# Kernel tuning notes

Measured on AMD Instinct MI355X. Metric: run time of the kernel, lower is better.

Reference implementation:

```python
import jax, jax.numpy as jnp
import numpy as np

LMAX = 4
S2_DIM = (LMAX + 1) ** 2                                  # 25: s2 irreps, mul 1 per l
SO3_DIM = sum((2 * l + 1) ** 2 for l in range(LMAX + 1))  # 165: so3 irreps, mul 2l+1 per l
B = 2048
F_S2, F_SO3 = 1, 16
N_S2_KERNEL = 48      # s2_healpix_grid(rec_level=1)
N_SO3_KERNEL = 192    # so3_near_identity_grid()
N_ACT_GRID = 4000     # SO3Activation resolution=10, aspect_ratio=2 -> 20x10x20, flattened
N_EVAL = 4608         # so3_healpix_grid(rec_level=2): 192 pixels x 24 gamma


def setup_inputs() -> dict:
    ks = jax.random.split(jax.random.key(0), 7)
    return {
        "x": jax.random.normal(ks[0], (B, F_S2, S2_DIM), jnp.float32),
        "w_s2": jax.random.normal(ks[1], (F_S2, F_SO3, N_S2_KERNEL), jnp.float32),
        "Y": jax.random.normal(ks[2], (N_S2_KERNEL, S2_DIM), jnp.float32),
        "w_so3": jax.random.normal(ks[3], (F_SO3, 1, N_SO3_KERNEL), jnp.float32),
        "D_kernel": jax.random.normal(ks[4], (N_SO3_KERNEL, SO3_DIM), jnp.float32),
        "D_act": jax.random.normal(ks[5], (N_ACT_GRID, SO3_DIM), jnp.float32),
        "eval_wigners": jax.random.normal(ks[6], (SO3_DIM, N_EVAL), jnp.float32) / np.sqrt(SO3_DIM),
    }


def _s2_to_so3_linear(x, psi):
    # e3nn o3.Linear(s2_irreps -> so3_irreps, f_in, f_out, external weights)
    # x:   [B, f_in, 25]  (mul 1 per degree l)
    # psi: [f_in, f_out, 25] ; column l^2+j is the weight to output-multiplicity j of degree l
    f_in, f_out = psi.shape[0], psi.shape[1]
    out, s = [], 0
    for l in range(LMAX + 1):
        d = 2 * l + 1
        x_l = x[..., s:s + d]                       # [B, f_in, d]
        p_l = psi[..., s:s + d]                     # [f_in, f_out, d] (j = out-mul idx)
        o = jnp.einsum('bxm,xyj->byjm', x_l, p_l) / np.sqrt(f_in)
        out.append(o.reshape(x.shape[0], f_out, d * d))
        s += d
    return jnp.concatenate(out, axis=-1)            # [B, f_out, 165]


def _so3_to_so3_linear(x, psi):
    # e3nn o3.Linear(so3_irreps -> so3_irreps, f_in, f_out, external weights)
    # x:   [B, f_in, 165] ; psi: [f_in, f_out, 165]
    f_in, f_out = psi.shape[0], psi.shape[1]
    out, s = [], 0
    for l in range(LMAX + 1):
        d = 2 * l + 1
        x_l = x[..., s:s + d * d].reshape(x.shape[0], f_in, d, d)   # [B,f_in,u,m]
        p_l = psi[..., s:s + d * d].reshape(f_in, f_out, d, d)      # [f_in,f_out,u,v]
        o = jnp.einsum('bxum,xyuv->byvm', x_l, p_l) / np.sqrt(f_in * d)
        out.append(o.reshape(x.shape[0], f_out, d * d))
        s += d * d
    return jnp.concatenate(out, axis=-1)            # [B, f_out, 165]


def _forward(x, w_s2, Y, w_so3, D_kernel, D_act, eval_wigners):
    # --- S2Convolution: kernel = SH-transform of grid weights, then irrep-wise linear
    psi1 = jnp.einsum('ni,xyn->xyi', Y, w_s2) / np.sqrt(N_S2_KERNEL)     # [1,16,25]
    h = _s2_to_so3_linear(x, psi1)                                        # [B,16,165]
    # --- SO3Activation: Fourier -> SO(3) grid -> relu -> Fourier
    g = jnp.einsum('bfi,gi->bfg', h, D_act) / np.sqrt(SO3_DIM)            # [B,16,4000]
    g = jax.nn.relu(g)
    h = jnp.einsum('bfg,gi->bfi', g, D_act) * (np.sqrt(SO3_DIM) / N_ACT_GRID)
    # --- SO3Convolution
    psi2 = jnp.einsum('ni,xyn->xyi', D_kernel, w_so3) / np.sqrt(N_SO3_KERNEL)  # [16,1,165]
    harmonics = _so3_to_so3_linear(h, psi2)                               # [B,1,165]
    # --- compute_probabilities: matmul with eval Wigner-D basis + softmax over grid
    probs = jax.nn.softmax(jnp.einsum('bfi,ie->be', harmonics, eval_wigners), axis=1)  # [B,4608]
    # --- top-k masking: zero out everything below the 5th-highest prob of sample 0
    fifth = jax.lax.top_k(probs, 5)[0][0, 4]
    probs = jnp.where(probs < fifth, 0.0, probs)
    return harmonics, probs


def reference(x, w_s2, Y, w_so3, D_kernel, D_act, eval_wigners):
    return _forward(x, w_s2, Y, w_so3, D_kernel, D_act, eval_wigners)
```

## Files before the change

### kernel.cpp

```cpp
#include <hip/hip_runtime.h>

typedef short bf16x8 __attribute__((ext_vector_type(8)));
typedef float f32x16 __attribute__((ext_vector_type(16)));
typedef int   i32x4  __attribute__((ext_vector_type(4)));

#define INV_SQRT165 0.07784989441615349f
#define FINAL_SCALE 0.0032113081446662823f
#define ZERO16 ((f32x16){0.f,0.f,0.f,0.f,0.f,0.f,0.f,0.f,0.f,0.f,0.f,0.f,0.f,0.f,0.f,0.f})

__device__ __forceinline__ unsigned short f2bf(float f) {
  unsigned int u = __builtin_bit_cast(unsigned int, f);
  unsigned int r = (u + 0x7FFFu + ((u >> 16) & 1u)) >> 16;
  return (unsigned short)r;
}
__device__ __forceinline__ float bf2f(unsigned short h) {
  unsigned int u = ((unsigned int)h) << 16;
  return __builtin_bit_cast(float, u);
}

__device__ __forceinline__ void gl_lds16(const void* g, void* l) {
  __builtin_amdgcn_global_load_lds(
      (const __attribute__((address_space(1))) unsigned int*)(unsigned long long)g,
      (__attribute__((address_space(3))) unsigned int*)(unsigned int)(unsigned long long)l,
      16, 0, 0);
}

__device__ __forceinline__ void decode_i(int i, int& lv, int& rel) {
  if (i < 1)       { lv = 0; rel = i; }
  else if (i < 10) { lv = 1; rel = i - 1; }
  else if (i < 35) { lv = 2; rel = i - 10; }
  else if (i < 84) { lv = 3; rel = i - 35; }
  else             { lv = 4; rel = i - 84; }
}
__device__ __forceinline__ int divq(int rel, int lv) {
  const int mag[5] = {32768, 10923, 6554, 4682, 3641};
  return (rel * mag[lv]) >> 15;
}

__device__ __forceinline__ int gperm(int p) {
  int a = p & 3, hlp = (p >> 2) & 1, c = p >> 3;
  return ((c >> 1) << 4) + hlp * 8 + ((c & 1) << 2) + a;
}

__global__ __launch_bounds__(256) void prep_k(const float* __restrict__ Da,
                                              const float* __restrict__ ew,
                                              const float* __restrict__ Y,
                                              const float* __restrict__ w_s2,
                                              const float* __restrict__ Dk,
                                              const float* __restrict__ w_so3,
                                              unsigned short* __restrict__ e1pre,
                                              unsigned short* __restrict__ d2pre,
                                              unsigned short* __restrict__ ewpre,
                                              float* __restrict__ psi2) {
  __shared__ __align__(16) unsigned short lds[13824];
  const int tid = threadIdx.x;
  const int l = tid & 63, hl = l >> 5, ln = l & 31;
  if (blockIdx.x < 512) {
    const int ci = blockIdx.x >> 2, yg = blockIdx.x & 3;
    const int g0 = ci * 32;
    float* psi1L = (float*)(lds + 6464);
    for (int e = tid; e < 6400; e += 256) lds[e] = 0;
    for (int e = tid; e < 400; e += 256) {
      int yv = e / 25, iv = e % 25;
      float s = 0.f;
      for (int n = 0; n < 48; n++) s += Y[n * 25 + iv] * w_s2[yv * 48 + n];
      psi1L[e] = s * 0.14433756729740643f;
    }
    __syncthreads();
    int rows = 4000 - g0; if (rows > 32) rows = 32; if (rows < 0) rows = 0;
    int ne = rows * 165;
    for (int e = tid; e < ne; e += 256) {
      int gl_ = e / 165, k = e - gl_ * 165;
      lds[gl_ * 200 + k] = f2bf(Da[g0 * 165 + e]);
    }
    __syncthreads();
    if (yg == 0) {
#pragma unroll
      for (int it = 0; it < 3; it++) {
        int tt = it * 4 + (tid >> 6);
        int nf = tt >> 1, gk = tt & 1;
        unsigned short v[8];
#pragma unroll
        for (int j = 0; j < 8; j++)
          v[j] = lds[(gk * 16 + hl * 8 + j) * 200 + nf * 32 + ln];
        *(i32x4*)(d2pre + ci * 6144 + tt * 512 + l * 8) = *(i32x4*)v;
      }
    }
    for (int yi = 0; yi < 4; yi++) {
      int yy = yg * 4 + yi;
#pragma unroll
      for (int it = 0; it < 4; it++) {
        int idx = it * 256 + tid;
        int kf = idx >> 9, r2 = idx & 511;
        int ll = r2 >> 3, j = r2 & 7;
        int lnn = ll & 31, hll = ll >> 5;
        int k = kf * 16 + hll * 8 + j;
        unsigned short ov = 0;
        if (k < 25) {
          int lv = (k < 1) ? 0 : (k < 4) ? 1 : (k < 9) ? 2 : (k < 16) ? 3 : 4;
          int d = 2 * lv + 1;
          int m = k - lv * lv;
          int off165 = lv * (4 * lv * lv - 1) / 3;
          int gp = gperm(lnn);
          float s = 0.f;
          const float* pr = psi1L + yy * 25 + lv * lv;
          const unsigned short* dr = lds + gp * 200 + off165 + m;
          for (int j2 = 0; j2 < d; j2++) s += pr[j2] * bf2f(dr[j2 * d]);
          ov = f2bf(s * INV_SQRT165);
        }
        e1pre[((yy * 128 + ci) * 2 + kf) * 512 + ll * 8 + j] = ov;
      }
    }
  } else if (blockIdx.x < 584) {
    const int bx2 = blockIdx.x - 512;
    const int n0 = bx2 * 64;
    for (int e = tid; e < 13824; e += 256) lds[e] = 0;
    __syncthreads();
    for (int e = tid; e < 10560; e += 256) {
      int k = e >> 6, n = e & 63;
      lds[k * 72 + n] = f2bf(ew[k * 4608 + n0 + n]);
    }
    __syncthreads();
#pragma unroll
    for (int it = 0; it < 6; it++) {
      int tb = it * 4 + (tid >> 6);
      int nt2 = tb / 12, kf = tb - nt2 * 12;
      unsigned short v[8];
#pragma unroll
      for (int j = 0; j < 8; j++)
        v[j] = lds[(kf * 16 + hl * 8 + j) * 72 + nt2 * 32 + ln];
      *(i32x4*)(ewpre + (bx2 * 2 + nt2) * 6144 + kf * 512 + l * 8) = *(i32x4*)v;
    }
  } else {
    int t = (blockIdx.x - 584) * 256 + tid;
    if (t < 2640) {
      int ch = t / 165, i = t % 165;
      float s = 0.f;
      for (int n = 0; n < 192; n++) s += Dk[n * 165 + i] * w_so3[ch * 192 + n];
      psi2[t] = s * (0.07216878364870323f * FINAL_SCALE);
    }
  }
}

__global__ __launch_bounds__(256, 2) void fused_mlp_k(
    const float* __restrict__ x,
    const unsigned short* __restrict__ e1pre,
    const unsigned short* __restrict__ d2pre,
    unsigned short* __restrict__ part)
{
  __shared__ __align__(16) unsigned char smem[24576];
  const int tid = threadIdx.x;
  const int w = tid >> 6, l = tid & 63;
  const int hl = l >> 5, ln = l & 31;
  const int h = blockIdx.x >> 8;
  const int y = (blockIdx.x >> 4) & 15;
  const int btq = blockIdx.x & 15;
  const int btp = w & 1, nh = w >> 1;
  const int bt0 = btq * 4 + btp * 2;
  const int c0 = h * 63;
  const int cnt = h ? 62 : 63;

  bf16x8 xf0[2], xf1[2];
#pragma unroll
  for (int t = 0; t < 2; t++) {
    const float* xr = x + ((bt0 + t) * 32 + ln) * 25;
#pragma unroll
    for (int kf = 0; kf < 2; kf++) {
      unsigned short v[8];
#pragma unroll
      for (int j = 0; j < 8; j++) {
        int k = kf * 16 + hl * 8 + j;
        v[j] = (k < 25) ? f2bf(xr[k]) : (unsigned short)0;
      }
      if (t == 0) xf0[kf] = *(bf16x8*)v; else xf1[kf] = *(bf16x8*)v;
    }
  }

  f32x16 o0[3], o1[3];
#pragma unroll
  for (int i = 0; i < 3; i++) { o0[i] = ZERO16; o1[i] = ZERO16; }

  const unsigned short* ebase = e1pre + (y * 128) * 1024;

  bf16x8 eC0 = *(const bf16x8*)(ebase + (c0 * 2 + 0) * 512 + l * 8);
  bf16x8 eC1 = *(const bf16x8*)(ebase + (c0 * 2 + 1) * 512 + l * 8);
#pragma unroll
  for (int i = 0; i < 3; i++) {
    int tb = w + i * 4;
    gl_lds16(d2pre + c0 * 6144 + tb * 512 + l * 8, smem + tb * 1024);
  }

  for (int ci = 0; ci < cnt; ci++) {
    __syncthreads();
    const unsigned char* cb = smem + (ci & 1) * 12288;
    bf16x8 eN0 = eC0, eN1 = eC1;
    if (ci + 1 < cnt) {
      unsigned char* nb = smem + ((ci + 1) & 1) * 12288;
      const int c = c0 + ci + 1;
#pragma unroll
      for (int i = 0; i < 3; i++) {
        int tb = w + i * 4;
        gl_lds16(d2pre + c * 6144 + tb * 512 + l * 8, nb + tb * 1024);
      }
      eN0 = *(const bf16x8*)(ebase + (c * 2 + 0) * 512 + l * 8);
      eN1 = *(const bf16x8*)(ebase + (c * 2 + 1) * 512 + l * 8);
    }
    f32x16 s0 = ZERO16, s1 = ZERO16;
    s0 = __builtin_amdgcn_mfma_f32_32x32x16_bf16(eC0, xf0[0], s0, 0, 0, 0);
    s1 = __builtin_amdgcn_mfma_f32_32x32x16_bf16(eC0, xf1[0], s1, 0, 0, 0);
    s0 = __builtin_amdgcn_mfma_f32_32x32x16_bf16(eC1, xf0[1], s0, 0, 0, 0);
    s1 = __builtin_amdgcn_mfma_f32_32x32x16_bf16(eC1, xf1[1], s1, 0, 0, 0);
    unsigned int dw0[8], dw1[8];
#pragma unroll
    for (int p = 0; p < 8; p++) {
      float lo = fmaxf(s0[2 * p], 0.f), hi = fmaxf(s0[2 * p + 1], 0.f);
      asm("v_cvt_pk_bf16_f32 %0, %1, %2" : "=v"(dw0[p]) : "v"(lo), "v"(hi));
      float lo1 = fmaxf(s1[2 * p], 0.f), hi1 = fmaxf(s1[2 * p + 1], 0.f);
      asm("v_cvt_pk_bf16_f32 %0, %1, %2" : "=v"(dw1[p]) : "v"(lo1), "v"(hi1));
    }
    bf16x8 a0[2], a1[2];
    a0[0] = __builtin_bit_cast(bf16x8, (i32x4){(int)dw0[0], (int)dw0[1], (int)dw0[2], (int)dw0[3]});
    a0[1] = __builtin_bit_cast(bf16x8, (i32x4){(int)dw0[4], (int)dw0[5], (int)dw0[6], (int)dw0[7]});
    a1[0] = __builtin_bit_cast(bf16x8, (i32x4){(int)dw1[0], (int)dw1[1], (int)dw1[2], (int)dw1[3]});
    a1[1] = __builtin_bit_cast(bf16x8, (i32x4){(int)dw1[4], (int)dw1[5], (int)dw1[6], (int)dw1[7]});
#pragma unroll
    for (int gk = 0; gk < 2; gk++) {
#pragma unroll
      for (int nf = 0; nf < 3; nf++) {
        bf16x8 b2 = *(const bf16x8*)(cb + ((nh * 3 + nf) * 2 + gk) * 1024 + l * 16);
        o0[nf] = __builtin_amdgcn_mfma_f32_32x32x16_bf16(a0[gk], b2, o0[nf], 0, 0, 0);
        o1[nf] = __builtin_amdgcn_mfma_f32_32x32x16_bf16(a1[gk], b2, o1[nf], 0, 0, 0);
      }
    }
    eC0 = eN0; eC1 = eN1;
  }

#pragma unroll
  for (int t = 0; t < 2; t++) {
    unsigned short* pp = part + (size_t)((h * 16 + y) * 2048 + (bt0 + t) * 32) * 192;
#pragma unroll
    for (int nf = 0; nf < 3; nf++) {
      int n = nh * 96 + nf * 32 + ln;
      if (n < 176) {
#pragma unroll
        for (int r = 0; r < 16; r++) {
          int row = (r & 3) + 8 * (r >> 2) + 4 * hl;
          float v = t ? o1[nf][r] : o0[nf][r];
          pp[row * 192 + n] = f2bf(v);
        }
      }
    }
  }
}

__global__ __launch_bounds__(256) void so3_k(const unsigned short* __restrict__ part,
                                             const float* __restrict__ psi2,
                                             float* __restrict__ harm_out,
                                             unsigned short* __restrict__ harmbpre) {
  __shared__ float lds[4 * 16 * 180];
  __shared__ float p2s[2640];
  const int tid = threadIdx.x;
  const int b0 = blockIdx.x * 4;
  for (int e = tid; e < 2640; e += 256) p2s[e] = psi2[e];
  {
    const int ybl = tid >> 2;
    const int yy = ybl & 15, bloc = ybl >> 4;
    const int s = tid & 3;
    const unsigned int* r0 = (const unsigned int*)(part + ((size_t)(0 * 16 + yy) * 2048 + b0 + bloc) * 192);
    const unsigned int* r1 = (const unsigned int*)(part + ((size_t)(1 * 16 + yy) * 2048 + b0 + bloc) * 192);
    float* dst = lds + (bloc * 16 + yy) * 180;
#pragma unroll
    for (int t = 0; t < 22; t++) {
      int d = s * 22 + t;
      if (d < 88) {
        unsigned int u0 = r0[d], u1 = r1[d];
        int n0 = d * 2;
        dst[n0]     = bf2f((unsigned short)(u0 & 0xFFFF)) + bf2f((unsigned short)(u1 & 0xFFFF));
        dst[n0 + 1] = bf2f((unsigned short)(u0 >> 16)) + bf2f((unsigned short)(u1 >> 16));
      }
    }
  }
  __syncthreads();
  for (int jj = tid; jj < 768; jj += 256) {
    int e = (jj * 683) >> 17;
    int i = jj - e * 192;
    int bb = b0 + e;
    unsigned short* hb = harmbpre + (((bb >> 5) * 12 + (i >> 4)) << 9)
                       + ((i >> 3) & 1) * 256 + (bb & 31) * 8 + (i & 7);
    if (i < 165) {
      const float* row0 = lds + e * (16 * 180);
      int lv, rel; decode_i(i, lv, rel);
      int d = 2 * lv + 1;
      int off = i - rel;
      int v = divq(rel, lv), m = rel - v * d;
      float s = 0.f;
      for (int ch = 0; ch < 16; ch++) {
        const float* rw = row0 + ch * 180 + off;
        const float* p2 = p2s + ch * 165 + off;
        for (int u = 0; u < d; u++) s += rw[u * d + m] * p2[u * d + v];
      }
      s *= 0.25f * rsqrtf((float)d);
      harm_out[bb * 165 + i] = s;
      *hb = f2bf(s);
    } else {
      *hb = 0;
    }
  }
}

__global__ __launch_bounds__(64) void eval_k(
    const unsigned short* __restrict__ harmbpre,
    const unsigned short* __restrict__ ewpre,
    float* __restrict__ logits,
    float* __restrict__ logit0)
{
  const int l = threadIdx.x;
  const int hl = l >> 5, ln = l & 31;
  const int mt = blockIdx.y;
  const int n0 = blockIdx.x * 192;

  bf16x8 a[12];
  const short* ap = (const short*)harmbpre + mt * 6144 + l * 8;
#pragma unroll
  for (int kf = 0; kf < 12; kf++) a[kf] = *(const bf16x8*)(ap + kf * 512);

  f32x16 acc[6];
#pragma unroll
  for (int nf = 0; nf < 6; nf++) acc[nf] = ZERO16;

  const short* bp = (const short*)ewpre + (blockIdx.x * 6) * 6144 + l * 8;
#pragma unroll
  for (int kf = 0; kf < 12; kf++) {
#pragma unroll
    for (int nf = 0; nf < 6; nf++) {
      bf16x8 b = *(const bf16x8*)(bp + nf * 6144 + kf * 512);
      acc[nf] = __builtin_amdgcn_mfma_f32_32x32x16_bf16(a[kf], b, acc[nf], 0, 0, 0);
    }
  }
#pragma unroll
  for (int nf = 0; nf < 6; nf++) {
    const int col = n0 + nf * 32 + ln;
#pragma unroll
    for (int r = 0; r < 16; r++) {
      int row = (r & 3) + 8 * (r >> 2) + 4 * hl;
      logits[(mt * 32 + row) * 4608 + col] = acc[nf][r];
    }
  }
  if (mt == 0 && hl == 0) {
#pragma unroll
    for (int nf = 0; nf < 6; nf++) logit0[n0 + nf * 32 + ln] = acc[nf][0];
  }
}

__global__ __launch_bounds__(256) void fifth_k(const float* __restrict__ logit0,
                                               float* __restrict__ fifth) {
  __shared__ float buf[4608];
  __shared__ float sm[4], ss[4];
  __shared__ float wv[4]; __shared__ int wi[4];
  __shared__ float gbest;
  const int tid = threadIdx.x;
  const int l = tid & 63, w = tid >> 6;
  float v[18];
  float mx = -3.4e38f;
#pragma unroll
  for (int i = 0; i < 18; i++) {
    v[i] = logit0[i * 256 + tid];
    buf[i * 256 + tid] = v[i];
    mx = fmaxf(mx, v[i]);
  }
#pragma unroll
  for (int off = 32; off >= 1; off >>= 1) mx = fmaxf(mx, __shfl_xor(mx, off));
  if (l == 0) sm[w] = mx;
  __syncthreads();
  mx = fmaxf(fmaxf(sm[0], sm[1]), fmaxf(sm[2], sm[3]));
  float s = 0.f;
#pragma unroll
  for (int i = 0; i < 18; i++) s += __expf(v[i] - mx);
#pragma unroll
  for (int off = 32; off >= 1; off >>= 1) s += __shfl_xor(s, off);
  if (l == 0) ss[w] = s;
  __syncthreads();
  s = ss[0] + ss[1] + ss[2] + ss[3];
  float inv = 1.f / s;

  float ff = 0.f;
  for (int it = 0; it < 5; it++) {
    float bm = -3.4e38f; int bi = 0;
    for (int i = tid; i < 4608; i += 256) {
      float xx = buf[i];
      if (xx > bm) { bm = xx; bi = i; }
    }
    for (int off = 32; off >= 1; off >>= 1) {
      float ov = __shfl_xor(bm, off); int oi = __shfl_xor(bi, off);
      if (ov > bm) { bm = ov; bi = oi; }
    }
    if (l == 0) { wv[w] = bm; wi[w] = bi; }
    __syncthreads();
    if (tid == 0) {
      float B = wv[0]; int I = wi[0];
      for (int k = 1; k < 4; k++) if (wv[k] > B) { B = wv[k]; I = wi[k]; }
      gbest = B;
      buf[I] = -3.4e38f;
    }
    __syncthreads();
    ff = gbest;
    __syncthreads();
  }
  if (tid == 0) *fifth = __expf(ff - mx) * inv;
}

__global__ __launch_bounds__(256) void smthresh_k(float* __restrict__ probs,
                                                  const float* __restrict__ fifth) {
  float* p = probs + (size_t)blockIdx.x * 4608;
  const int tid = threadIdx.x;
  const int l = tid & 63, w = tid >> 6;
  __shared__ float sm[4], ss[4];
  float v[18];
  float mx = -3.4e38f;
#pragma unroll
  for (int i = 0; i < 18; i++) { v[i] = p[i * 256 + tid]; mx = fmaxf(mx, v[i]); }
#pragma unroll
  for (int off = 32; off >= 1; off >>= 1) mx = fmaxf(mx, __shfl_xor(mx, off));
  if (l == 0) sm[w] = mx;
  __syncthreads();
  mx = fmaxf(fmaxf(sm[0], sm[1]), fmaxf(sm[2], sm[3]));
  float s = 0.f;
#pragma unroll
  for (int i = 0; i < 18; i++) { v[i] = __expf(v[i] - mx); s += v[i]; }
#pragma unroll
  for (int off = 32; off >= 1; off >>= 1) s += __shfl_xor(s, off);
  if (l == 0) ss[w] = s;
  __syncthreads();
  s = ss[0] + ss[1] + ss[2] + ss[3];
  float inv = 1.f / s;
  float t = *fifth;
#pragma unroll
  for (int i = 0; i < 18; i++) {
    float pv = v[i] * inv;
    p[i * 256 + tid] = (pv < t) ? 0.f : pv;
  }
}

extern "C" void kernel_launch(void* const* d_in, const int* in_sizes, int n_in,
                              void* d_out, int out_size, void* d_ws, size_t ws_size,
                              hipStream_t stream) {
  const float* x     = (const float*)d_in[0];
  const float* w_s2  = (const float*)d_in[1];
  const float* Y     = (const float*)d_in[2];
  const float* w_so3 = (const float*)d_in[3];
  const float* Dk    = (const float*)d_in[4];
  const float* Da    = (const float*)d_in[5];
  const float* ew    = (const float*)d_in[6];

  float* out = (float*)d_out;
  float* harm_out = out;
  float* probs    = out + 337920;
  unsigned short* part = (unsigned short*)probs;

  char* ws = (char*)d_ws;
  float* psi2  = (float*)(ws + 0);
  float* fifth = (float*)(ws + 10560);
  unsigned short* e1pre    = (unsigned short*)(ws + 12288);
  unsigned short* d2pre    = (unsigned short*)(ws + 4206592);
  unsigned short* ewpre    = (unsigned short*)(ws + 5779456);
  unsigned short* harmbpre = (unsigned short*)(ws + 7548928);
  float* logit0 = (float*)(ws + 8335360);

  prep_k<<<595, 256, 0, stream>>>(Da, ew, Y, w_s2, Dk, w_so3, e1pre, d2pre, ewpre, psi2);
  fused_mlp_k<<<512, 256, 0, stream>>>(x, e1pre, d2pre, part);
  so3_k<<<512, 256, 0, stream>>>(part, psi2, harm_out, harmbpre);
  eval_k<<<dim3(24, 64), 64, 0, stream>>>(harmbpre, ewpre, probs, logit0);
  fifth_k<<<1, 256, 0, stream>>>(logit0, fifth);
  smthresh_k<<<2048, 256, 0, stream>>>(probs, fifth);
}
```

Before: 220.5 us.

## Double block size in fused MLP and stage e1 tiles through LDS

The fused MLP kernel now runs 256 blocks of 512 threads (8 waves) instead of 512 blocks of 256. Each block covers 8 batch tiles, so every d2 and e1 chunk staged in LDS is shared by twice as many waves, which halves redundant global reads of the weights. The e1 fragments, previously loaded per wave straight into registers, are now fetched asynchronously into the double-buffered LDS alongside d2. The trade-off is fewer, larger blocks, a somewhat larger LDS footprint, and a barrier that has to synchronise 8 waves.

```diff
diff --git a/kernel.cpp b/kernel.cpp
--- a/kernel.cpp
+++ b/kernel.cpp
@@ -142,21 +142,21 @@
   }
 }
 
-__global__ __launch_bounds__(256, 2) void fused_mlp_k(
+__global__ __launch_bounds__(512, 2) void fused_mlp_k(
     const float* __restrict__ x,
     const unsigned short* __restrict__ e1pre,
     const unsigned short* __restrict__ d2pre,
     unsigned short* __restrict__ part)
 {
-  __shared__ __align__(16) unsigned char smem[24576];
+  __shared__ __align__(16) unsigned char smem[28672];
   const int tid = threadIdx.x;
   const int w = tid >> 6, l = tid & 63;
   const int hl = l >> 5, ln = l & 31;
-  const int h = blockIdx.x >> 8;
-  const int y = (blockIdx.x >> 4) & 15;
-  const int btq = blockIdx.x & 15;
-  const int btp = w & 1, nh = w >> 1;
-  const int bt0 = btq * 4 + btp * 2;
+  const int h = blockIdx.x >> 7;
+  const int y = (blockIdx.x >> 3) & 15;
+  const int btG = blockIdx.x & 7;
+  const int btsub = w >> 1, nh = w & 1;
+  const int bt0 = btG * 8 + btsub * 2;
   const int c0 = h * 63;
   const int cnt = h ? 62 : 63;
 
@@ -182,29 +182,36 @@
 
   const unsigned short* ebase = e1pre + (y * 128) * 1024;
 
-  bf16x8 eC0 = *(const bf16x8*)(ebase + (c0 * 2 + 0) * 512 + l * 8);
-  bf16x8 eC1 = *(const bf16x8*)(ebase + (c0 * 2 + 1) * 512 + l * 8);
-#pragma unroll
-  for (int i = 0; i < 3; i++) {
-    int tb = w + i * 4;
-    gl_lds16(d2pre + c0 * 6144 + tb * 512 + l * 8, smem + tb * 1024);
+#pragma unroll
+  for (int i = 0; i < 2; i++) {
+    int tb = w + i * 8;
+    if (tb < 14) {
+      const unsigned short* src = (tb < 2)
+          ? ebase + c0 * 1024 + tb * 512 + l * 8
+          : d2pre + c0 * 6144 + (tb - 2) * 512 + l * 8;
+      gl_lds16(src, smem + tb * 1024);
+    }
   }
 
   for (int ci = 0; ci < cnt; ci++) {
     __syncthreads();
-    const unsigned char* cb = smem + (ci & 1) * 12288;
-    bf16x8 eN0 = eC0, eN1 = eC1;
+    const unsigned char* cb = smem + (ci & 1) * 14336;
     if (ci + 1 < cnt) {
-      unsigned char* nb = smem + ((ci + 1) & 1) * 12288;
+      unsigned char* nb = smem + ((ci + 1) & 1) * 14336;
       const int c = c0 + ci + 1;
 #pragma unroll
-      for (int i = 0; i < 3; i++) {
-        int tb = w + i * 4;
-        gl_lds16(d2pre + c * 6144 + tb * 512 + l * 8, nb + tb * 1024);
-      }
-      eN0 = *(const bf16x8*)(ebase + (c * 2 + 0) * 512 + l * 8);
-      eN1 = *(const bf16x8*)(ebase + (c * 2 + 1) * 512 + l * 8);
-    }
+      for (int i = 0; i < 2; i++) {
+        int tb = w + i * 8;
+        if (tb < 14) {
+          const unsigned short* src = (tb < 2)
+              ? ebase + c * 1024 + tb * 512 + l * 8
+              : d2pre + c * 6144 + (tb - 2) * 512 + l * 8;
+          gl_lds16(src, nb + tb * 1024);
+        }
+      }
+    }
+    bf16x8 eC0 = *(const bf16x8*)(cb + l * 16);
+    bf16x8 eC1 = *(const bf16x8*)(cb + 1024 + l * 16);
     f32x16 s0 = ZERO16, s1 = ZERO16;
     s0 = __builtin_amdgcn_mfma_f32_32x32x16_bf16(eC0, xf0[0], s0, 0, 0, 0);
     s1 = __builtin_amdgcn_mfma_f32_32x32x16_bf16(eC0, xf1[0], s1, 0, 0, 0);
@@ -213,8 +220,8 @@
     unsigned int dw0[8], dw1[8];
 #pragma unroll
     for (int p = 0; p < 8; p++) {
-      float lo = fmaxf(s0[2 * p], 0.f), hi = fmaxf(s0[2 * p + 1], 0.f);
-      asm("v_cvt_pk_bf16_f32 %0, %1, %2" : "=v"(dw0[p]) : "v"(lo), "v"(hi));
+      float lo0 = fmaxf(s0[2 * p], 0.f), hi0 = fmaxf(s0[2 * p + 1], 0.f);
+      asm("v_cvt_pk_bf16_f32 %0, %1, %2" : "=v"(dw0[p]) : "v"(lo0), "v"(hi0));
       float lo1 = fmaxf(s1[2 * p], 0.f), hi1 = fmaxf(s1[2 * p + 1], 0.f);
       asm("v_cvt_pk_bf16_f32 %0, %1, %2" : "=v"(dw1[p]) : "v"(lo1), "v"(hi1));
     }
@@ -227,12 +234,11 @@
     for (int gk = 0; gk < 2; gk++) {
 #pragma unroll
       for (int nf = 0; nf < 3; nf++) {
-        bf16x8 b2 = *(const bf16x8*)(cb + ((nh * 3 + nf) * 2 + gk) * 1024 + l * 16);
+        bf16x8 b2 = *(const bf16x8*)(cb + 2048 + ((nh * 3 + nf) * 2 + gk) * 1024 + l * 16);
         o0[nf] = __builtin_amdgcn_mfma_f32_32x32x16_bf16(a0[gk], b2, o0[nf], 0, 0, 0);
         o1[nf] = __builtin_amdgcn_mfma_f32_32x32x16_bf16(a1[gk], b2, o1[nf], 0, 0, 0);
       }
     }
-    eC0 = eN0; eC1 = eN1;
   }
 
 #pragma unroll
@@ -467,7 +473,7 @@
   float* logit0 = (float*)(ws + 8335360);
 
   prep_k<<<595, 256, 0, stream>>>(Da, ew, Y, w_s2, Dk, w_so3, e1pre, d2pre, ewpre, psi2);
-  fused_mlp_k<<<512, 256, 0, stream>>>(x, e1pre, d2pre, part);
+  fused_mlp_k<<<256, 512, 0, stream>>>(x, e1pre, d2pre, part);
   so3_k<<<512, 256, 0, stream>>>(part, psi2, harm_out, harmbpre);
   eval_k<<<dim3(24, 64), 64, 0, stream>>>(harmbpre, ewpre, probs, logit0);
   fifth_k<<<1, 256, 0, stream>>>(logit0, fifth);
```

Measured after the change: 216.3 us. No clear change (-1.9%).
